# Optimization experiments

Hardware: AMD Instinct MI355X
Metric: run time of the kernel (lower is better)

The kernel has to match this reference:

```python
import jax, jax.numpy as jnp
import numpy as np

B, H, T, D = 2, 16, 2048, 64


def setup_inputs() -> dict:
    key = jax.random.key(0)
    kq, kk, kv, km = jax.random.split(key, 4)
    q = jax.random.normal(kq, (B, H, T, D), dtype=jnp.float32)
    k = jax.random.normal(kk, (B, H, T, D), dtype=jnp.float32)
    v = jax.random.normal(kv, (B, H, T, D), dtype=jnp.float32)
    mask = jax.random.randint(km, (T, T), 0, 2, dtype=jnp.int32)
    return {"q": q, "k": k, "v": v, "mask": mask}


def reference(q, k, v, mask):
    d_k = q.shape[-1]
    scale = jnp.asarray(d_k, q.dtype) ** -0.5
    # (B,H,T,D) @ (B,H,D,T) -> (B,H,T,T)
    scores = jnp.einsum("bhtd,bhsd->bhts", q * scale, k)
    # mask broadcast over (B,H); masked positions set to -1e9 as in torch code
    scores = jnp.where(mask[None, None, :, :] == 0, jnp.asarray(-1e9, scores.dtype), scores)
    attn = jax.nn.softmax(scores, axis=-1)
    # (B,H,T,T) @ (B,H,T,D) -> (B,H,T,D)
    out = jnp.einsum("bhts,bhsd->bhtd", attn, v)
    return (out, attn)
```

## Files before the change

### kernel.cpp

```cpp
#include <hip/hip_runtime.h>
#include <hip/hip_bf16.h>
#include <cstddef>

#define T_SEQ 2048
#define D_HEAD 64
#define BC 64
#define NKT (T_SEQ / BC)
#define PAD 72

typedef __bf16 bf16x8 __attribute__((ext_vector_type(8)));
typedef float f32x4 __attribute__((ext_vector_type(4)));
typedef unsigned short u16x8 __attribute__((ext_vector_type(8)));

__device__ __forceinline__ unsigned short f2bf(float f) {
  __bf16 h = (__bf16)f;
  return __builtin_bit_cast(unsigned short, h);
}
__device__ __forceinline__ bf16x8 ldfrag(const unsigned short* p) {
  u16x8 t = *(const u16x8*)p;
  return __builtin_bit_cast(bf16x8, t);
}
__device__ __forceinline__ f32x4 mfma16(bf16x8 a, bf16x8 b, f32x4 c) {
  return __builtin_amdgcn_mfma_f32_16x16x32_bf16(a, b, c, 0, 0, 0);
}
__device__ __forceinline__ void bar_sync() {
  asm volatile("" ::: "memory");
  __builtin_amdgcn_s_barrier();
  asm volatile("" ::: "memory");
}
__device__ __forceinline__ void lds_fence() {
  asm volatile("s_waitcnt lgkmcnt(0)" ::: "memory");
}
__device__ __forceinline__ float exp2_hw(float x) { return __builtin_amdgcn_exp2f(x); }
__device__ __forceinline__ float log2_hw(float x) { return __builtin_amdgcn_logf(x); }

__global__ __launch_bounds__(256) void mask_pack(const int* __restrict__ maskg,
                                                 unsigned* __restrict__ mp) {
  const size_t total = (size_t)T_SEQ * T_SEQ;
  size_t idx = (size_t)blockIdx.x * blockDim.x + threadIdx.x;
  const size_t stride = (size_t)gridDim.x * blockDim.x;
  const int lane = threadIdx.x & 63;
  for (; idx < total; idx += stride) {
    int mv = maskg[idx];
    unsigned long long b = __ballot(mv != 0);
    if (lane == 0)       mp[idx >> 5] = (unsigned)b;
    else if (lane == 32) mp[idx >> 5] = (unsigned)(b >> 32);
  }
}

__global__ __launch_bounds__(256, 4) void attn_fused2(
    const float* __restrict__ qg, const float* __restrict__ kg,
    const float* __restrict__ vg, const unsigned* __restrict__ mpk,
    float* __restrict__ outg, float* __restrict__ attng)
{
  __shared__ unsigned short ks[BC][PAD];
  __shared__ unsigned short vt[D_HEAD][PAD];
  __shared__ unsigned short ps[64][PAD];

  const int bid = blockIdx.x;
  const int lin = (bid & 7) * 128 + (bid >> 3);
  const int bh  = lin >> 5;
  const int strip = lin & 31;

  const int tid  = threadIdx.x;
  const int lane = tid & 63;
  const int wid  = tid >> 6;
  const int lr = lane & 15, lh = lane >> 4;
  const int r0 = strip * 64 + wid * 16;
  const int sv = tid >> 2;
  const int sc4 = (tid & 3) << 4;
  const int vt7 = tid & 7;
  const int vs2 = (tid >> 3) * 2;

  const float C = 0.18033688011112042f;
  const float* qb = qg + (size_t)bh * T_SEQ * D_HEAD;
  const float* kb = kg + (size_t)bh * T_SEQ * D_HEAD;
  const float* vb = vg + (size_t)bh * T_SEQ * D_HEAD;
  const int ROWW = T_SEQ / 32;
  const f32x4 zero4 = {0.f, 0.f, 0.f, 0.f};

  bf16x8 qf[2];
  {
    const float* qr = qb + (size_t)(r0 + lr) * D_HEAD;
    #pragma unroll
    for (int kk = 0; kk < 2; ++kk) {
      float4 a = *(const float4*)(qr + kk * 32 + lh * 8);
      float4 b = *(const float4*)(qr + kk * 32 + lh * 8 + 4);
      u16x8 u;
      u[0] = f2bf(a.x); u[1] = f2bf(a.y); u[2] = f2bf(a.z); u[3] = f2bf(a.w);
      u[4] = f2bf(b.x); u[5] = f2bf(b.y); u[6] = f2bf(b.z); u[7] = f2bf(b.w);
      qf[kk] = __builtin_bit_cast(bf16x8, u);
    }
  }

  f32x4 acc[4];
  #pragma unroll
  for (int nt = 0; nt < 4; ++nt) acc[nt] = zero4;
  float psum_s = 0.f;

  for (int kt = 0; kt < NKT; ++kt) {
    const int n0 = kt * BC;
    bar_sync();
    {
      const float* ksrc = kb + (size_t)(n0 + sv) * D_HEAD + sc4;
      float4 k0 = *(const float4*)(ksrc + 0),  k1 = *(const float4*)(ksrc + 4);
      float4 k2 = *(const float4*)(ksrc + 8),  k3 = *(const float4*)(ksrc + 12);
      u16x8 w0, w1;
      w0[0]=f2bf(k0.x); w0[1]=f2bf(k0.y); w0[2]=f2bf(k0.z); w0[3]=f2bf(k0.w);
      w0[4]=f2bf(k1.x); w0[5]=f2bf(k1.y); w0[6]=f2bf(k1.z); w0[7]=f2bf(k1.w);
      w1[0]=f2bf(k2.x); w1[1]=f2bf(k2.y); w1[2]=f2bf(k2.z); w1[3]=f2bf(k2.w);
      w1[4]=f2bf(k3.x); w1[5]=f2bf(k3.y); w1[6]=f2bf(k3.z); w1[7]=f2bf(k3.w);
      *(u16x8*)&ks[sv][sc4 + 0] = w0;
      *(u16x8*)&ks[sv][sc4 + 8] = w1;
    }
    {
      const float* v0 = vb + (size_t)(n0 + vs2) * D_HEAD + vt7;
      const float* v1 = v0 + D_HEAD;
      #pragma unroll
      for (int j = 0; j < 8; ++j) {
        const float a = v0[8 * j];
        const float b = v1[8 * j];
        const unsigned w = (unsigned)f2bf(a) | ((unsigned)f2bf(b) << 16);
        *(unsigned*)&vt[vt7 + 8 * j][vs2] = w;
      }
    }
    const unsigned mw0 = mpk[(size_t)(r0 + lr) * ROWW + kt * 2];
    const unsigned mw1 = mpk[(size_t)(r0 + lr) * ROWW + kt * 2 + 1];
    lds_fence(); bar_sync();

    f32x4 st[4];
    #pragma unroll
    for (int nt = 0; nt < 4; ++nt) st[nt] = zero4;
    #pragma unroll
    for (int kk = 0; kk < 2; ++kk) {
      bf16x8 kf[4];
      #pragma unroll
      for (int nt = 0; nt < 4; ++nt) kf[nt] = ldfrag(&ks[nt * 16 + lr][kk * 32 + lh * 8]);
      #pragma unroll
      for (int nt = 0; nt < 4; ++nt) st[nt] = mfma16(kf[nt], qf[kk], st[nt]);
    }
    #pragma unroll
    for (int nt = 0; nt < 4; ++nt) {
      const unsigned w = (nt & 2) ? mw1 : mw0;
      float p[4];
      #pragma unroll
      for (int r = 0; r < 4; ++r) {
        const int bit = (nt & 1) * 16 + 4 * lh + r;
        p[r] = ((w >> bit) & 1) ? exp2_hw(st[nt][r] * C) : 0.f;
        psum_s += p[r];
      }
      uint2 u;
      u.x = (unsigned)f2bf(p[0]) | ((unsigned)f2bf(p[1]) << 16);
      u.y = (unsigned)f2bf(p[2]) | ((unsigned)f2bf(p[3]) << 16);
      *(uint2*)&ps[wid * 16 + lr][nt * 16 + 4 * lh] = u;
    }
    lds_fence();
    #pragma unroll
    for (int kk = 0; kk < 2; ++kk) {
      const bf16x8 pa = ldfrag(&ps[wid * 16 + lr][kk * 32 + lh * 8]);
      #pragma unroll
      for (int nt = 0; nt < 4; ++nt) {
        const bf16x8 vf = ldfrag(&vt[nt * 16 + lr][kk * 32 + lh * 8]);
        acc[nt] = mfma16(pa, vf, acc[nt]);
      }
    }
  }

  psum_s += __shfl_xor(psum_s, 16);
  psum_s += __shfl_xor(psum_s, 32);
  const float iv_s = 1.0f / psum_s;
  float ivq[4], lg2ivq[4];
  #pragma unroll
  for (int r = 0; r < 4; ++r) {
    ivq[r] = __shfl(iv_s, 4 * lh + r);
    lg2ivq[r] = log2_hw(ivq[r]);
  }

  float* ob = outg + (size_t)(bh * T_SEQ + r0) * D_HEAD;
  #pragma unroll
  for (int nt = 0; nt < 4; ++nt)
    #pragma unroll
    for (int r = 0; r < 4; ++r)
      ob[(size_t)(4 * lh + r) * D_HEAD + nt * 16 + lr] = acc[nt][r] * ivq[r];

  float* ab = attng + (size_t)(bh * T_SEQ + r0) * T_SEQ;
  for (int kt = 0; kt < NKT; ++kt) {
    const int n0 = kt * BC;
    bar_sync();
    {
      const float* ksrc = kb + (size_t)(n0 + sv) * D_HEAD + sc4;
      float4 k0 = *(const float4*)(ksrc + 0),  k1 = *(const float4*)(ksrc + 4);
      float4 k2 = *(const float4*)(ksrc + 8),  k3 = *(const float4*)(ksrc + 12);
      u16x8 w0, w1;
      w0[0]=f2bf(k0.x); w0[1]=f2bf(k0.y); w0[2]=f2bf(k0.z); w0[3]=f2bf(k0.w);
      w0[4]=f2bf(k1.x); w0[5]=f2bf(k1.y); w0[6]=f2bf(k1.z); w0[7]=f2bf(k1.w);
      w1[0]=f2bf(k2.x); w1[1]=f2bf(k2.y); w1[2]=f2bf(k2.z); w1[3]=f2bf(k2.w);
      w1[4]=f2bf(k3.x); w1[5]=f2bf(k3.y); w1[6]=f2bf(k3.z); w1[7]=f2bf(k3.w);
      *(u16x8*)&ks[sv][sc4 + 0] = w0;
      *(u16x8*)&ks[sv][sc4 + 8] = w1;
    }
    unsigned mw[4][2];
    #pragma unroll
    for (int r = 0; r < 4; ++r) {
      const size_t mrow = (size_t)(r0 + 4 * lh + r) * ROWW + kt * 2;
      mw[r][0] = mpk[mrow];
      mw[r][1] = mpk[mrow + 1];
    }
    lds_fence(); bar_sync();

    f32x4 sc_[4];
    #pragma unroll
    for (int nt = 0; nt < 4; ++nt) sc_[nt] = zero4;
    #pragma unroll
    for (int kk = 0; kk < 2; ++kk) {
      bf16x8 kf[4];
      #pragma unroll
      for (int nt = 0; nt < 4; ++nt) kf[nt] = ldfrag(&ks[nt * 16 + lr][kk * 32 + lh * 8]);
      #pragma unroll
      for (int nt = 0; nt < 4; ++nt) sc_[nt] = mfma16(qf[kk], kf[nt], sc_[nt]);
    }
    #pragma unroll
    for (int r = 0; r < 4; ++r) {
      float* arow = ab + (size_t)(4 * lh + r) * T_SEQ + n0;
      #pragma unroll
      for (int nt = 0; nt < 4; ++nt) {
        const int mv = (mw[r][nt >> 1] >> ((nt & 1) * 16 + lr)) & 1;
        const float p = mv ? exp2_hw(__builtin_fmaf(sc_[nt][r], C, lg2ivq[r])) : 0.f;
        __builtin_nontemporal_store(p, arow + nt * 16 + lr);
      }
    }
  }
}

__global__ __launch_bounds__(512, 2) void attn_fused_fb(
    const float* __restrict__ qg, const float* __restrict__ kg,
    const float* __restrict__ vg, const int* __restrict__ maskg,
    float* __restrict__ outg, float* __restrict__ attng)
{
  __shared__ unsigned short qs[128][PAD];
  __shared__ unsigned short ks[64][PAD];
  __shared__ unsigned short vt[64][PAD];
  __shared__ unsigned short pp[128][PAD];
  __shared__ float rsum[128];
  int bid = blockIdx.x;
  int lin = (bid & 7) * 64 + (bid >> 3);
  int bh = lin >> 4, br0 = (lin & 15) * 128;
  const int tid = threadIdx.x, lane = tid & 63, wid = tid >> 6;
  const int wm = wid >> 1, wn = wid & 1, lr = lane & 15, lh = lane >> 4;
  const float scale = 0.125f;
  const float* qb = qg + ((size_t)bh * T_SEQ + br0) * D_HEAD;
  const float* kbp = kg + (size_t)bh * T_SEQ * D_HEAD;
  const float* vbp = vg + (size_t)bh * T_SEQ * D_HEAD;
  if (tid < 128) rsum[tid] = 0.f;
  #pragma unroll
  for (int it = 0; it < 4; ++it) {
    int idx = it * 512 + tid;
    int r = idx >> 4, c = (idx & 15) << 2;
    float4 f = *(const float4*)(qb + (size_t)r * D_HEAD + c);
    *(ushort4*)&qs[r][c] = make_ushort4(f2bf(f.x), f2bf(f.y), f2bf(f.z), f2bf(f.w));
  }
  f32x4 acc_o[2][2];
  const f32x4 zero4 = {0.f, 0.f, 0.f, 0.f};
  #pragma unroll
  for (int a = 0; a < 2; ++a)
    #pragma unroll
    for (int b = 0; b < 2; ++b) acc_o[a][b] = zero4;
  float psum[2][4] = {{0.f,0.f,0.f,0.f},{0.f,0.f,0.f,0.f}};
  __syncthreads();
  for (int kt = 0; kt < NKT; ++kt) {
    const int kb0 = kt * 64;
    #pragma unroll
    for (int it = 0; it < 2; ++it) {
      int idx = it * 512 + tid;
      int r = idx >> 4, c = (idx & 15) << 2;
      float4 f = *(const float4*)(kbp + (size_t)(kb0 + r) * D_HEAD + c);
      *(ushort4*)&ks[r][c] = make_ushort4(f2bf(f.x), f2bf(f.y), f2bf(f.z), f2bf(f.w));
      float4 g = *(const float4*)(vbp + (size_t)(kb0 + r) * D_HEAD + c);
      vt[c+0][r] = f2bf(g.x); vt[c+1][r] = f2bf(g.y);
      vt[c+2][r] = f2bf(g.z); vt[c+3][r] = f2bf(g.w);
    }
    __syncthreads();
    f32x4 sc[2][2];
    #pragma unroll
    for (int a = 0; a < 2; ++a)
      #pragma unroll
      for (int b = 0; b < 2; ++b) sc[a][b] = zero4;
    #pragma unroll
    for (int kk = 0; kk < 2; ++kk) {
      const int ke = kk * 32 + lh * 8;
      bf16x8 af[2], bfq[2];
      #pragma unroll
      for (int mt = 0; mt < 2; ++mt) af[mt] = ldfrag(&qs[wm*32 + mt*16 + lr][ke]);
      #pragma unroll
      for (int nt = 0; nt < 2; ++nt) bfq[nt] = ldfrag(&ks[wn*32 + nt*16 + lr][ke]);
      #pragma unroll
      for (int mt = 0; mt < 2; ++mt)
        #pragma unroll
        for (int nt = 0; nt < 2; ++nt)
          sc[mt][nt] = mfma16(af[mt], bfq[nt], sc[mt][nt]);
    }
    #pragma unroll
    for (int mt = 0; mt < 2; ++mt)
      #pragma unroll
      for (int nt = 0; nt < 2; ++nt)
        #pragma unroll
        for (int r = 0; r < 4; ++r) {
          int row = wm*32 + mt*16 + lh*4 + r, col = wn*32 + nt*16 + lr;
          int mv = maskg[(size_t)(br0 + row) * T_SEQ + (kb0 + col)];
          float p = mv ? __expf(sc[mt][nt][r] * scale) : 0.f;
          psum[mt][r] += p;
          pp[row][col] = f2bf(p);
        }
    __syncthreads();
    #pragma unroll
    for (int kk = 0; kk < 2; ++kk) {
      const int ke = kk * 32 + lh * 8;
      bf16x8 pa[2], vf[2];
      #pragma unroll
      for (int mt = 0; mt < 2; ++mt) pa[mt] = ldfrag(&pp[wm*32 + mt*16 + lr][ke]);
      #pragma unroll
      for (int nt = 0; nt < 2; ++nt) vf[nt] = ldfrag(&vt[wn*32 + nt*16 + lr][ke]);
      #pragma unroll
      for (int mt = 0; mt < 2; ++mt)
        #pragma unroll
        for (int nt = 0; nt < 2; ++nt)
          acc_o[mt][nt] = mfma16(pa[mt], vf[nt], acc_o[mt][nt]);
    }
    __syncthreads();
  }
  #pragma unroll
  for (int mt = 0; mt < 2; ++mt)
    #pragma unroll
    for (int r = 0; r < 4; ++r) {
      float sv = psum[mt][r];
      sv += __shfl_xor(sv, 1); sv += __shfl_xor(sv, 2);
      sv += __shfl_xor(sv, 4); sv += __shfl_xor(sv, 8);
      if (lr == 0) atomicAdd(&rsum[wm*32 + mt*16 + lh*4 + r], sv);
    }
  __syncthreads();
  float invs[2][4];
  #pragma unroll
  for (int mt = 0; mt < 2; ++mt)
    #pragma unroll
    for (int r = 0; r < 4; ++r)
      invs[mt][r] = 1.0f / rsum[wm*32 + mt*16 + lh*4 + r];
  float* ob = outg + ((size_t)bh * T_SEQ + br0) * D_HEAD;
  #pragma unroll
  for (int mt = 0; mt < 2; ++mt)
    #pragma unroll
    for (int nt = 0; nt < 2; ++nt)
      #pragma unroll
      for (int r = 0; r < 4; ++r) {
        int row = wm*32 + mt*16 + lh*4 + r, col = wn*32 + nt*16 + lr;
        ob[(size_t)row * D_HEAD + col] = acc_o[mt][nt][r] * invs[mt][r];
      }
  float* ab = attng + (size_t)bh * T_SEQ * T_SEQ + (size_t)br0 * T_SEQ;
  for (int kt = 0; kt < NKT; ++kt) {
    const int kb0 = kt * 64;
    __syncthreads();
    #pragma unroll
    for (int it = 0; it < 2; ++it) {
      int idx = it * 512 + tid;
      int r = idx >> 4, c = (idx & 15) << 2;
      float4 f = *(const float4*)(kbp + (size_t)(kb0 + r) * D_HEAD + c);
      *(ushort4*)&ks[r][c] = make_ushort4(f2bf(f.x), f2bf(f.y), f2bf(f.z), f2bf(f.w));
    }
    __syncthreads();
    f32x4 sc[2][2];
    #pragma unroll
    for (int a = 0; a < 2; ++a)
      #pragma unroll
      for (int b = 0; b < 2; ++b) sc[a][b] = zero4;
    #pragma unroll
    for (int kk = 0; kk < 2; ++kk) {
      const int ke = kk * 32 + lh * 8;
      bf16x8 af[2], bfq[2];
      #pragma unroll
      for (int mt = 0; mt < 2; ++mt) af[mt] = ldfrag(&qs[wm*32 + mt*16 + lr][ke]);
      #pragma unroll
      for (int nt = 0; nt < 2; ++nt) bfq[nt] = ldfrag(&ks[wn*32 + nt*16 + lr][ke]);
      #pragma unroll
      for (int mt = 0; mt < 2; ++mt)
        #pragma unroll
        for (int nt = 0; nt < 2; ++nt)
          sc[mt][nt] = mfma16(af[mt], bfq[nt], sc[mt][nt]);
    }
    #pragma unroll
    for (int mt = 0; mt < 2; ++mt)
      #pragma unroll
      for (int nt = 0; nt < 2; ++nt)
        #pragma unroll
        for (int r = 0; r < 4; ++r) {
          int row = wm*32 + mt*16 + lh*4 + r, col = wn*32 + nt*16 + lr;
          int mv = maskg[(size_t)(br0 + row) * T_SEQ + (kb0 + col)];
          float p = mv ? __expf(sc[mt][nt][r] * scale) * invs[mt][r] : 0.f;
          ab[(size_t)row * T_SEQ + kb0 + col] = p;
        }
  }
}

extern "C" void kernel_launch(void* const* d_in, const int* in_sizes, int n_in,
                              void* d_out, int out_size, void* d_ws, size_t ws_size,
                              hipStream_t stream) {
  const float* q = (const float*)d_in[0];
  const float* k = (const float*)d_in[1];
  const float* v = (const float*)d_in[2];
  const int* mask = (const int*)d_in[3];
  float* out = (float*)d_out;
  float* attn = out + (size_t)2 * 16 * T_SEQ * D_HEAD;

  const size_t mpk_bytes = (size_t)T_SEQ * T_SEQ / 8;
  if (ws_size >= mpk_bytes) {
    unsigned* mp = (unsigned*)d_ws;
    mask_pack<<<dim3(2048), 256, 0, stream>>>(mask, mp);
    attn_fused2<<<dim3(1024), 256, 0, stream>>>(q, k, v, mp, out, attn);
  } else {
    attn_fused_fb<<<dim3(512), 512, 0, stream>>>(q, k, v, mask, out, attn);
  }
}
```

Measured before the change: 192.2 us.

## Precompute bf16 K and transposed bf16 V in a prep kernel

Adds a kv_prep kernel that converts K to bf16 and V to a transposed bf16 layout once, writing both into workspace. The main attention kernel then loads these with wide 16-byte copies into LDS instead of loading fp32 and converting per tile, which was repeated by every one of the 32 strips per head and done twice for K (once per pass). This halves the K/V bytes the main kernel reads and removes the strided scalar V transpose. The cost is an extra kernel launch, extra workspace, and a global round trip for the converted data. If the workspace is too small, the code falls back to the old path.

After: 203.8 us. 1.06x slower.

```diff
diff --git a/kernel.cpp b/kernel.cpp
--- a/kernel.cpp
+++ b/kernel.cpp
@@ -48,9 +48,45 @@
   }
 }
 
-__global__ __launch_bounds__(256, 4) void attn_fused2(
-    const float* __restrict__ qg, const float* __restrict__ kg,
-    const float* __restrict__ vg, const unsigned* __restrict__ mpk,
+__global__ __launch_bounds__(256) void kv_prep(const float* __restrict__ kg,
+                                               const float* __restrict__ vg,
+                                               unsigned short* __restrict__ kbf,
+                                               unsigned short* __restrict__ vtw) {
+  const int b = blockIdx.x, tid = threadIdx.x;
+  if (b < 1024) {
+    const int head = b >> 5, rb = (b & 31) * 64;
+    const float* src = kg + ((size_t)head * T_SEQ + rb) * D_HEAD;
+    unsigned short* dst = kbf + ((size_t)head * T_SEQ + rb) * D_HEAD;
+    const int row = tid >> 2, c = (tid & 3) * 16;
+    const float* s = src + (size_t)row * D_HEAD + c;
+    u16x8 lo, hi;
+    #pragma unroll
+    for (int j = 0; j < 8; ++j) { lo[j] = f2bf(s[j]); hi[j] = f2bf(s[j + 8]); }
+    *(u16x8*)(dst + (size_t)row * D_HEAD + c)     = lo;
+    *(u16x8*)(dst + (size_t)row * D_HEAD + c + 8) = hi;
+  } else {
+    __shared__ float lds[64][68];
+    const int b2 = b - 1024;
+    const int head = b2 >> 5, st = (b2 & 31) * 64;
+    const float* src = vg + ((size_t)head * T_SEQ + st) * D_HEAD;
+    const int srow = tid >> 2, dbase = (tid & 3) * 16;
+    #pragma unroll
+    for (int j = 0; j < 4; ++j)
+      *(float4*)&lds[srow][dbase + j * 4] = *(const float4*)(src + (size_t)srow * D_HEAD + dbase + j * 4);
+    __syncthreads();
+    const int d = tid >> 2, s8 = (tid & 3) * 16;
+    u16x8 lo, hi;
+    #pragma unroll
+    for (int j = 0; j < 8; ++j) { lo[j] = f2bf(lds[s8 + j][d]); hi[j] = f2bf(lds[s8 + 8 + j][d]); }
+    unsigned short* dst = vtw + ((size_t)head * D_HEAD + d) * T_SEQ + st + s8;
+    *(u16x8*)dst       = lo;
+    *(u16x8*)(dst + 8) = hi;
+  }
+}
+
+__global__ __launch_bounds__(256, 4) void attn_fused7(
+    const float* __restrict__ qg, const unsigned short* __restrict__ kbf,
+    const unsigned short* __restrict__ vtw, const unsigned* __restrict__ mpk,
     float* __restrict__ outg, float* __restrict__ attng)
 {
   __shared__ unsigned short ks[BC][PAD];
@@ -69,13 +105,11 @@
   const int r0 = strip * 64 + wid * 16;
   const int sv = tid >> 2;
   const int sc4 = (tid & 3) << 4;
-  const int vt7 = tid & 7;
-  const int vs2 = (tid >> 3) * 2;
 
   const float C = 0.18033688011112042f;
   const float* qb = qg + (size_t)bh * T_SEQ * D_HEAD;
-  const float* kb = kg + (size_t)bh * T_SEQ * D_HEAD;
-  const float* vb = vg + (size_t)bh * T_SEQ * D_HEAD;
+  const unsigned short* kb2 = kbf + (size_t)bh * T_SEQ * D_HEAD;
+  const unsigned short* vb2 = vtw + (size_t)bh * D_HEAD * T_SEQ;
   const int ROWW = T_SEQ / 32;
   const f32x4 zero4 = {0.f, 0.f, 0.f, 0.f};
 
@@ -102,27 +136,14 @@
     const int n0 = kt * BC;
     bar_sync();
     {
-      const float* ksrc = kb + (size_t)(n0 + sv) * D_HEAD + sc4;
-      float4 k0 = *(const float4*)(ksrc + 0),  k1 = *(const float4*)(ksrc + 4);
-      float4 k2 = *(const float4*)(ksrc + 8),  k3 = *(const float4*)(ksrc + 12);
-      u16x8 w0, w1;
-      w0[0]=f2bf(k0.x); w0[1]=f2bf(k0.y); w0[2]=f2bf(k0.z); w0[3]=f2bf(k0.w);
-      w0[4]=f2bf(k1.x); w0[5]=f2bf(k1.y); w0[6]=f2bf(k1.z); w0[7]=f2bf(k1.w);
-      w1[0]=f2bf(k2.x); w1[1]=f2bf(k2.y); w1[2]=f2bf(k2.z); w1[3]=f2bf(k2.w);
-      w1[4]=f2bf(k3.x); w1[5]=f2bf(k3.y); w1[6]=f2bf(k3.z); w1[7]=f2bf(k3.w);
-      *(u16x8*)&ks[sv][sc4 + 0] = w0;
-      *(u16x8*)&ks[sv][sc4 + 8] = w1;
+      const unsigned short* ksrc = kb2 + (size_t)(n0 + sv) * D_HEAD + sc4;
+      *(u16x8*)&ks[sv][sc4 + 0] = *(const u16x8*)(ksrc + 0);
+      *(u16x8*)&ks[sv][sc4 + 8] = *(const u16x8*)(ksrc + 8);
     }
     {
-      const float* v0 = vb + (size_t)(n0 + vs2) * D_HEAD + vt7;
-      const float* v1 = v0 + D_HEAD;
-      #pragma unroll
-      for (int j = 0; j < 8; ++j) {
-        const float a = v0[8 * j];
-        const float b = v1[8 * j];
-        const unsigned w = (unsigned)f2bf(a) | ((unsigned)f2bf(b) << 16);
-        *(unsigned*)&vt[vt7 + 8 * j][vs2] = w;
-      }
+      const unsigned short* vsrc = vb2 + (size_t)sv * T_SEQ + n0 + sc4;
+      *(u16x8*)&vt[sv][sc4 + 0] = *(const u16x8*)(vsrc + 0);
+      *(u16x8*)&vt[sv][sc4 + 8] = *(const u16x8*)(vsrc + 8);
     }
     const unsigned mw0 = mpk[(size_t)(r0 + lr) * ROWW + kt * 2];
     const unsigned mw1 = mpk[(size_t)(r0 + lr) * ROWW + kt * 2 + 1];
@@ -188,16 +209,9 @@
     const int n0 = kt * BC;
     bar_sync();
     {
-      const float* ksrc = kb + (size_t)(n0 + sv) * D_HEAD + sc4;
-      float4 k0 = *(const float4*)(ksrc + 0),  k1 = *(const float4*)(ksrc + 4);
-      float4 k2 = *(const float4*)(ksrc + 8),  k3 = *(const float4*)(ksrc + 12);
-      u16x8 w0, w1;
-      w0[0]=f2bf(k0.x); w0[1]=f2bf(k0.y); w0[2]=f2bf(k0.z); w0[3]=f2bf(k0.w);
-      w0[4]=f2bf(k1.x); w0[5]=f2bf(k1.y); w0[6]=f2bf(k1.z); w0[7]=f2bf(k1.w);
-      w1[0]=f2bf(k2.x); w1[1]=f2bf(k2.y); w1[2]=f2bf(k2.z); w1[3]=f2bf(k2.w);
-      w1[4]=f2bf(k3.x); w1[5]=f2bf(k3.y); w1[6]=f2bf(k3.z); w1[7]=f2bf(k3.w);
-      *(u16x8*)&ks[sv][sc4 + 0] = w0;
-      *(u16x8*)&ks[sv][sc4 + 8] = w1;
+      const unsigned short* ksrc = kb2 + (size_t)(n0 + sv) * D_HEAD + sc4;
+      *(u16x8*)&ks[sv][sc4 + 0] = *(const u16x8*)(ksrc + 0);
+      *(u16x8*)&ks[sv][sc4 + 8] = *(const u16x8*)(ksrc + 8);
     }
     unsigned mw[4][2];
     #pragma unroll
@@ -410,10 +424,15 @@
   float* attn = out + (size_t)2 * 16 * T_SEQ * D_HEAD;
 
   const size_t mpk_bytes = (size_t)T_SEQ * T_SEQ / 8;
-  if (ws_size >= mpk_bytes) {
+  const size_t kbf_bytes = (size_t)32 * T_SEQ * D_HEAD * 2;
+  const size_t vt_bytes  = kbf_bytes;
+  if (ws_size >= mpk_bytes + kbf_bytes + vt_bytes) {
     unsigned* mp = (unsigned*)d_ws;
+    unsigned short* kbf = (unsigned short*)((char*)d_ws + mpk_bytes);
+    unsigned short* vtw = (unsigned short*)((char*)d_ws + mpk_bytes + kbf_bytes);
     mask_pack<<<dim3(2048), 256, 0, stream>>>(mask, mp);
-    attn_fused2<<<dim3(1024), 256, 0, stream>>>(q, k, v, mp, out, attn);
+    kv_prep<<<dim3(2048), 256, 0, stream>>>(k, v, kbf, vtw);
+    attn_fused7<<<dim3(1024), 256, 0, stream>>>(q, kbf, vtw, mp, out, attn);
   } else {
     attn_fused_fb<<<dim3(512), 512, 0, stream>>>(q, k, v, mask, out, attn);
   }
```
